# Optimization experiments

Measured on AMD Instinct MI355X. Metric: run time of the kernel, lower is better.

The kernel has to match this reference:

```python
import jax, jax.numpy as jnp
import numpy as np

B, T, C, H = 256, 256, 384, 64  # batch, seq (== block_size), n_embd, head_size


def setup_inputs() -> dict:
    key = jax.random.key(0)
    kx, kk, kq, kv = jax.random.split(key, 4)
    scale = C ** -0.5
    x = jax.random.normal(kx, (B, T, C), dtype=jnp.float32)
    Wk = jax.random.normal(kk, (C, H), dtype=jnp.float32) * scale
    Wq = jax.random.normal(kq, (C, H), dtype=jnp.float32) * scale
    Wv = jax.random.normal(kv, (C, H), dtype=jnp.float32) * scale
    return {"x": x, "Wk": Wk, "Wq": Wq, "Wv": Wv}


def reference(x, Wk, Wq, Wv):
    # Single causal self-attention head (x_kv=None path). Dropout is eval-mode (identity).
    Tn = x.shape[1]
    k = x @ Wk            # [B, T, H]
    q = x @ Wq            # [B, T, H]
    v = x @ Wv            # [B, T, H]
    inv_sqrt_d = k.shape[-1] ** -0.5
    wei = jnp.einsum('bth,bsh->bts', q, k) * inv_sqrt_d  # [B, T, T]
    causal = jnp.tril(jnp.ones((Tn, Tn), dtype=bool))
    wei = jnp.where(causal, wei, -jnp.inf)
    wei = jax.nn.softmax(wei, axis=-1)
    out = jnp.einsum('bts,bsh->bth', wei, v)             # [B, T, H]
    return out
```

## Files before the change

kernel.cpp:

```cpp
#include <hip/hip_runtime.h>

#define BATCH 256
#define SEQ   256
#define CDIM  384
#define HDIM  64

typedef __attribute__((ext_vector_type(8))) short bf16x8;
typedef __attribute__((ext_vector_type(4))) float f32x4;

__device__ __forceinline__ unsigned f2bf(float f) {
  union { float f; unsigned u; } v; v.f = f;
  unsigned r = v.u + 0x7FFFu + ((v.u >> 16) & 1u);
  return r >> 16;
}

__global__ void wtrans_kernel(const float* __restrict__ Wk, const float* __restrict__ Wq,
                              const float* __restrict__ Wv, unsigned short* __restrict__ WTf) {
  int gid = blockIdx.x * 256 + threadIdx.x;
  if (gid >= 192 * CDIM) return;
  int n = gid / CDIM, kk = gid - n * CDIM;
  const float* W = (n < 64) ? Wq : (n < 128) ? Wk : Wv;
  int nt = n >> 4, ln = n & 15, ks = kk >> 5, sub = (kk >> 3) & 3, j = kk & 7;
  int lane = ln + 16 * sub;
  WTf[(((size_t)ks * 12 + nt) * 64 + lane) * 8 + j] =
      (unsigned short)f2bf(W[kk * HDIM + (n & 63)]);
}

__global__ __launch_bounds__(1024, 4) void fused_kernel(
    const float* __restrict__ x, const unsigned short* __restrict__ WTf,
    float* __restrict__ out) {
  __shared__ __align__(16) unsigned short lds[73728];
  const int tid = threadIdx.x, b = blockIdx.x;
  const int w = tid >> 6, lane = tid & 63;
  const int ln15 = lane & 15, quad = lane >> 4;

  {
    const uint4* src = (const uint4*)WTf;
    #pragma unroll
    for (int i = 0; i < 9; ++i) {
      int c = i * 1024 + tid;
      __builtin_amdgcn_global_load_lds(
          (const __attribute__((address_space(1))) unsigned*)(src + c),
          (__attribute__((address_space(3))) unsigned*)((char*)lds + (size_t)c * 16),
          16, 0, 0);
    }
  }

  bf16x8 bx[12];
  {
    const float* xr = x + (size_t)(b * 256 + w * 16 + ln15) * CDIM + quad * 8;
    #pragma unroll
    for (int hh = 0; hh < 2; ++hh) {
      float4 A[12];
      #pragma unroll
      for (int j = 0; j < 6; ++j) {
        A[2 * j]     = *(const float4*)(xr + (hh * 6 + j) * 32);
        A[2 * j + 1] = *(const float4*)(xr + (hh * 6 + j) * 32 + 4);
      }
      #pragma unroll
      for (int j = 0; j < 6; ++j) {
        bf16x8 t;
        t[0] = (short)f2bf(A[2 * j].x);     t[1] = (short)f2bf(A[2 * j].y);
        t[2] = (short)f2bf(A[2 * j].z);     t[3] = (short)f2bf(A[2 * j].w);
        t[4] = (short)f2bf(A[2 * j + 1].x); t[5] = (short)f2bf(A[2 * j + 1].y);
        t[6] = (short)f2bf(A[2 * j + 1].z); t[7] = (short)f2bf(A[2 * j + 1].w);
        bx[hh * 6 + j] = t;
      }
    }
  }

  __syncthreads();

  f32x4 acc[12];
  #pragma unroll
  for (int nt = 0; nt < 12; ++nt) acc[nt] = (f32x4){0.f, 0.f, 0.f, 0.f};

  #pragma unroll
  for (int ks = 0; ks < 12; ++ks) {
    #pragma unroll
    for (int nt = 0; nt < 12; ++nt) {
      bf16x8 aw = *(const bf16x8*)&lds[((ks * 12 + nt) * 64 + lane) * 8];
      acc[nt] = __builtin_amdgcn_mfma_f32_16x16x32_bf16(aw, bx[ks], acc[nt], 0, 0, 0);
    }
  }

  __syncthreads();

  unsigned short (*QL)[72]  = (unsigned short(*)[72])lds;
  unsigned short (*KL)[72]  = (unsigned short(*)[72])(lds + 18432);
  unsigned short (*VT)[264] = (unsigned short(*)[264])(lds + 36864);
  unsigned short (*PL)[36]  = (unsigned short(*)[36])(lds + 53760 + w * 576);

  {
    const int trow = w * 16 + ln15;
    #pragma unroll
    for (int nt = 0; nt < 4; ++nt) {
      f32x4 a = acc[nt];
      unsigned p0 = f2bf(a[0]) | (f2bf(a[1]) << 16);
      unsigned p1 = f2bf(a[2]) | (f2bf(a[3]) << 16);
      *(uint2*)&QL[trow][nt * 16 + quad * 4] = (uint2){p0, p1};
    }
    #pragma unroll
    for (int nt = 4; nt < 8; ++nt) {
      f32x4 a = acc[nt];
      unsigned p0 = f2bf(a[0]) | (f2bf(a[1]) << 16);
      unsigned p1 = f2bf(a[2]) | (f2bf(a[3]) << 16);
      *(uint2*)&KL[trow][(nt - 4) * 16 + quad * 4] = (uint2){p0, p1};
    }
    #pragma unroll
    for (int nt = 8; nt < 12; ++nt) {
      f32x4 a = acc[nt];
      const int h = (nt - 8) * 16 + quad * 4;
      #pragma unroll
      for (int i = 0; i < 4; ++i)
        VT[h + i][trow] = (unsigned short)f2bf(a[i]);
    }
  }
  __syncthreads();

  {
    const int mt = w;
    const int t0 = mt * 16;
    const int NT = (mt | 1) + 1;

    bf16x8 aq[2];
    #pragma unroll
    for (int ks = 0; ks < 2; ++ks)
      aq[ks] = *(const bf16x8*)&QL[t0 + ln15][ks * 32 + quad * 8];

    float sv[16][4];
    #pragma unroll
    for (int nt = 0; nt < 16; ++nt) {
      if (nt < NT) {
        f32x4 a2 = (f32x4){0.f, 0.f, 0.f, 0.f};
        #pragma unroll
        for (int ks = 0; ks < 2; ++ks) {
          bf16x8 bf = *(const bf16x8*)&KL[nt * 16 + ln15][ks * 32 + quad * 8];
          a2 = __builtin_amdgcn_mfma_f32_16x16x32_bf16(aq[ks], bf, a2, 0, 0, 0);
        }
        int colg = nt * 16 + ln15;
        #pragma unroll
        for (int i = 0; i < 4; ++i) {
          int rowg = t0 + quad * 4 + i;
          sv[nt][i] = (colg <= rowg) ? a2[i] * 0.125f : -3.0e38f;
        }
      }
    }
    float mx[4] = {-3.0e38f, -3.0e38f, -3.0e38f, -3.0e38f};
    #pragma unroll
    for (int nt = 0; nt < 16; ++nt)
      if (nt < NT) {
        #pragma unroll
        for (int i = 0; i < 4; ++i) mx[i] = fmaxf(mx[i], sv[nt][i]);
      }
    #pragma unroll
    for (int i = 0; i < 4; ++i) {
      mx[i] = fmaxf(mx[i], __shfl_xor(mx[i], 8, 64));
      mx[i] = fmaxf(mx[i], __shfl_xor(mx[i], 4, 64));
      mx[i] = fmaxf(mx[i], __shfl_xor(mx[i], 2, 64));
      mx[i] = fmaxf(mx[i], __shfl_xor(mx[i], 1, 64));
    }
    float sm[4] = {0.f, 0.f, 0.f, 0.f};
    #pragma unroll
    for (int nt = 0; nt < 16; ++nt)
      if (nt < NT) {
        #pragma unroll
        for (int i = 0; i < 4; ++i) {
          float e = __expf(sv[nt][i] - mx[i]);
          sv[nt][i] = e;
          sm[i] += e;
        }
      }
    #pragma unroll
    for (int i = 0; i < 4; ++i) {
      sm[i] += __shfl_xor(sm[i], 8, 64);
      sm[i] += __shfl_xor(sm[i], 4, 64);
      sm[i] += __shfl_xor(sm[i], 2, 64);
      sm[i] += __shfl_xor(sm[i], 1, 64);
    }
    float inv[4];
    #pragma unroll
    for (int i = 0; i < 4; ++i) inv[i] = 1.0f / sm[i];

    f32x4 o[4];
    #pragma unroll
    for (int ont = 0; ont < 4; ++ont) o[ont] = (f32x4){0.f, 0.f, 0.f, 0.f};

    #pragma unroll
    for (int kc = 0; kc < 8; ++kc) {
      if (kc * 2 < NT) {
        #pragma unroll
        for (int half = 0; half < 2; ++half) {
          int nt = kc * 2 + half;
          #pragma unroll
          for (int i = 0; i < 4; ++i)
            PL[quad * 4 + i][half * 16 + ln15] =
                (unsigned short)f2bf(sv[nt][i] * inv[i]);
        }
        bf16x8 pa = *(const bf16x8*)&PL[ln15][quad * 8];
        #pragma unroll
        for (int ont = 0; ont < 4; ++ont) {
          bf16x8 vb = *(const bf16x8*)&VT[ont * 16 + ln15][kc * 32 + quad * 8];
          o[ont] = __builtin_amdgcn_mfma_f32_16x16x32_bf16(pa, vb, o[ont], 0, 0, 0);
        }
      }
    }

    #pragma unroll
    for (int ont = 0; ont < 4; ++ont) {
      int h = ont * 16 + ln15;
      #pragma unroll
      for (int i = 0; i < 4; ++i)
        out[(size_t)(b * 256 + t0 + quad * 4 + i) * HDIM + h] = o[ont][i];
    }
  }
}

extern "C" void kernel_launch(void* const* d_in, const int* in_sizes, int n_in,
                              void* d_out, int out_size, void* d_ws, size_t ws_size,
                              hipStream_t stream) {
  const float* x  = (const float*)d_in[0];
  const float* Wk = (const float*)d_in[1];
  const float* Wq = (const float*)d_in[2];
  const float* Wv = (const float*)d_in[3];
  float* out = (float*)d_out;

  unsigned short* WTf = (unsigned short*)d_ws;

  wtrans_kernel<<<(192 * CDIM + 255) / 256, 256, 0, stream>>>(Wk, Wq, Wv, WTf);
  fused_kernel<<<256, 1024, 0, stream>>>(x, WTf, out);
}
```

Measured before the change: 181.3 us.

## Stream x through LDS via async DMA and load projection weights in halves

Replaces the upfront register load and conversion of each wave's x rows with per-K-chunk asynchronous global-to-LDS copies. The copies are double-buffered in a swizzled per-wave staging area and interleaved with the QKV projection MFMAs. The bf16 weight tile is now loaded in two halves into a smaller LDS region, with a block barrier and full drain between halves. The goal is to overlap x fetch latency with compute and cut register pressure from holding all of x in registers. The cost is more manual waitcnt and barrier synchronisation, plus a stall when the second weight half is loaded.

```diff
diff --git a/kernel.cpp b/kernel.cpp
--- a/kernel.cpp
+++ b/kernel.cpp
@@ -29,60 +29,109 @@
 __global__ __launch_bounds__(1024, 4) void fused_kernel(
     const float* __restrict__ x, const unsigned short* __restrict__ WTf,
     float* __restrict__ out) {
-  __shared__ __align__(16) unsigned short lds[73728];
+  __shared__ __align__(16) unsigned short lds[69632];
   const int tid = threadIdx.x, b = blockIdx.x;
   const int w = tid >> 6, lane = tid & 63;
   const int ln15 = lane & 15, quad = lane >> 4;
 
   {
-    const uint4* src = (const uint4*)WTf;
-    #pragma unroll
-    for (int i = 0; i < 9; ++i) {
-      int c = i * 1024 + tid;
-      __builtin_amdgcn_global_load_lds(
-          (const __attribute__((address_space(1))) unsigned*)(src + c),
-          (__attribute__((address_space(3))) unsigned*)((char*)lds + (size_t)c * 16),
-          16, 0, 0);
-    }
-  }
-
-  bf16x8 bx[12];
-  {
-    const float* xr = x + (size_t)(b * 256 + w * 16 + ln15) * CDIM + quad * 8;
-    #pragma unroll
-    for (int hh = 0; hh < 2; ++hh) {
-      float4 A[12];
-      #pragma unroll
-      for (int j = 0; j < 6; ++j) {
-        A[2 * j]     = *(const float4*)(xr + (hh * 6 + j) * 32);
-        A[2 * j + 1] = *(const float4*)(xr + (hh * 6 + j) * 32 + 4);
-      }
-      #pragma unroll
-      for (int j = 0; j < 6; ++j) {
-        bf16x8 t;
-        t[0] = (short)f2bf(A[2 * j].x);     t[1] = (short)f2bf(A[2 * j].y);
-        t[2] = (short)f2bf(A[2 * j].z);     t[3] = (short)f2bf(A[2 * j].w);
-        t[4] = (short)f2bf(A[2 * j + 1].x); t[5] = (short)f2bf(A[2 * j + 1].y);
-        t[6] = (short)f2bf(A[2 * j + 1].z); t[7] = (short)f2bf(A[2 * j + 1].w);
-        bx[hh * 6 + j] = t;
-      }
-    }
-  }
-
-  __syncthreads();
+    #pragma unroll
+    for (int i = 0; i < 5; ++i) {
+      int m = i * 16 + w;
+      if (m < 72) {
+        int c = m * 64 + lane;
+        __builtin_amdgcn_global_load_lds(
+            (const __attribute__((address_space(1))) unsigned*)((const char*)WTf + (size_t)c * 16),
+            (__attribute__((address_space(3))) unsigned*)((char*)lds + (size_t)c * 16),
+            16, 0, 0);
+      }
+    }
+  }
+  __builtin_amdgcn_sched_barrier(0);
+
+  const int r0 = lane >> 3;
+  const int cgs = (lane & 7) ^ r0;
+  const char* xs0 = (const char*)x +
+      ((size_t)(b * 256 + w * 16 + r0) * CDIM + cgs * 4) * 4;
+  const char* xs1 = xs0 + (size_t)8 * CDIM * 4;
+  char* xld = (char*)lds + 73728 + w * 4096 + lane * 16;
+
+#define XDMA(K, S)                                                            \
+  __builtin_amdgcn_global_load_lds(                                           \
+      (const __attribute__((address_space(1))) unsigned*)(xs0 + (K) * 128),   \
+      (__attribute__((address_space(3))) unsigned*)(xld + (S) * 2048),        \
+      16, 0, 0);                                                              \
+  __builtin_amdgcn_global_load_lds(                                           \
+      (const __attribute__((address_space(1))) unsigned*)(xs1 + (K) * 128),   \
+      (__attribute__((address_space(3))) unsigned*)(xld + (S) * 2048 + 1024), \
+      16, 0, 0);
+
+  XDMA(0, 0)
+  __builtin_amdgcn_sched_barrier(0);
+  asm volatile("s_waitcnt vmcnt(2)" ::: "memory");
+  __builtin_amdgcn_s_barrier();
+  __builtin_amdgcn_sched_barrier(0);
+
+  const int roA = ln15 * 128 + (((2 * quad) ^ (ln15 & 7)) * 16);
+  const int roB = ln15 * 128 + ((((2 * quad) + 1) ^ (ln15 & 7)) * 16);
 
   f32x4 acc[12];
   #pragma unroll
   for (int nt = 0; nt < 12; ++nt) acc[nt] = (f32x4){0.f, 0.f, 0.f, 0.f};
 
-  #pragma unroll
-  for (int ks = 0; ks < 12; ++ks) {
-    #pragma unroll
-    for (int nt = 0; nt < 12; ++nt) {
-      bf16x8 aw = *(const bf16x8*)&lds[((ks * 12 + nt) * 64 + lane) * 8];
-      acc[nt] = __builtin_amdgcn_mfma_f32_16x16x32_bf16(aw, bx[ks], acc[nt], 0, 0, 0);
-    }
-  }
+#define PSTEP(K, KIDX, VMN, ISSUE)                                            \
+  {                                                                           \
+    ISSUE                                                                     \
+    __builtin_amdgcn_sched_barrier(0);                                        \
+    asm volatile("s_waitcnt vmcnt(" #VMN ")" ::: "memory");                   \
+    __builtin_amdgcn_sched_barrier(0);                                        \
+    const char* cb = (const char*)lds + 73728 + w * 4096 + ((K) & 1) * 2048;  \
+    float4 fa = *(const float4*)(cb + roA);                                   \
+    float4 fb = *(const float4*)(cb + roB);                                   \
+    bf16x8 t;                                                                 \
+    t[0] = (short)f2bf(fa.x); t[1] = (short)f2bf(fa.y);                       \
+    t[2] = (short)f2bf(fa.z); t[3] = (short)f2bf(fa.w);                       \
+    t[4] = (short)f2bf(fb.x); t[5] = (short)f2bf(fb.y);                       \
+    t[6] = (short)f2bf(fb.z); t[7] = (short)f2bf(fb.w);                       \
+    _Pragma("unroll")                                                         \
+    for (int nt = 0; nt < 12; ++nt) {                                         \
+      bf16x8 aw = *(const bf16x8*)&lds[(((KIDX) * 12 + nt) * 64 + lane) * 8]; \
+      acc[nt] = __builtin_amdgcn_mfma_f32_16x16x32_bf16(aw, t, acc[nt], 0, 0, 0); \
+    }                                                                         \
+  }
+
+  PSTEP(0, 0, 2, XDMA(1, 1))
+  PSTEP(1, 1, 2, XDMA(2, 0))
+  PSTEP(2, 2, 2, XDMA(3, 1))
+  PSTEP(3, 3, 2, XDMA(4, 0))
+  PSTEP(4, 4, 2, XDMA(5, 1))
+  PSTEP(5, 5, 2, XDMA(6, 0))
+
+  __builtin_amdgcn_sched_barrier(0);
+  __builtin_amdgcn_s_barrier();
+  {
+    #pragma unroll
+    for (int i = 0; i < 5; ++i) {
+      int m = i * 16 + w;
+      if (m < 72) {
+        int c = m * 64 + lane;
+        __builtin_amdgcn_global_load_lds(
+            (const __attribute__((address_space(1))) unsigned*)((const char*)WTf + 73728 + (size_t)c * 16),
+            (__attribute__((address_space(3))) unsigned*)((char*)lds + (size_t)c * 16),
+            16, 0, 0);
+      }
+    }
+  }
+  asm volatile("s_waitcnt vmcnt(0)" ::: "memory");
+  __builtin_amdgcn_s_barrier();
+  __builtin_amdgcn_sched_barrier(0);
+
+  PSTEP(6,  0, 2, XDMA(7, 1))
+  PSTEP(7,  1, 2, XDMA(8, 0))
+  PSTEP(8,  2, 2, XDMA(9, 1))
+  PSTEP(9,  3, 2, XDMA(10, 0))
+  PSTEP(10, 4, 2, XDMA(11, 1))
+  PSTEP(11, 5, 0, )
 
   __syncthreads();
 
```

New measurement: 169.4 us. -6.5%, faster.

## Split each batch across two 512-thread blocks with streamed weight tiles

Applied to the files above, without the earlier changes.

Launches two 512-thread blocks per batch element instead of one 1024-thread block. The lower block handles query rows 0-127, and the upper block handles rows 128-255, recomputing K/V for the lower rows itself. The full weight matrix is no longer staged in LDS up front; each k-slice of weights is streamed in through a small double-buffered LDS window with barriers, overlapped with prefetched x loads. Q stays in registers and goes through a per-wave scratch area instead of a shared Q tile. This is meant to balance the causal work and raise parallelism, at the cost of redundant projection work in the upper block and many more barriers.

```diff
diff --git a/kernel.cpp b/kernel.cpp
--- a/kernel.cpp
+++ b/kernel.cpp
@@ -26,107 +26,131 @@
       (unsigned short)f2bf(W[kk * HDIM + (n & 63)]);
 }
 
-__global__ __launch_bounds__(1024, 4) void fused_kernel(
+__global__ __launch_bounds__(512, 4) void fused_kernel(
     const float* __restrict__ x, const unsigned short* __restrict__ WTf,
     float* __restrict__ out) {
-  __shared__ __align__(16) unsigned short lds[73728];
-  const int tid = threadIdx.x, b = blockIdx.x;
+  __shared__ __align__(16) char L[77312];
+  const int tid = threadIdx.x, bid = blockIdx.x;
+  const int b = bid & 255;
+  const bool up = bid >= 256;
   const int w = tid >> 6, lane = tid & 63;
   const int ln15 = lane & 15, quad = lane >> 4;
 
+  unsigned short (*KL)[68]  = (unsigned short(*)[68])L;
+  unsigned short (*VT)[260] = (unsigned short(*)[260])(L + 34816);
+  unsigned short (*PLw)[36] = (unsigned short(*)[36])(L + 68096 + w * 1152);
+
+#define WDMA(GREC, LREC)                                                      \
+  __builtin_amdgcn_global_load_lds(                                           \
+      (const __attribute__((address_space(1))) unsigned*)((const char*)WTf +  \
+          (size_t)(GREC) * 1024 + lane * 16),                                 \
+      (__attribute__((address_space(3))) unsigned*)(L + (LREC) * 1024 + lane * 16), \
+      16, 0, 0);
+
+#define PROJPASS(ACC, NTB, NTC, XR)                                           \
+  {                                                                           \
+    float4 Qa[2], Qb[2];                                                      \
+    Qa[0] = *(const float4*)((XR) + 0);                                       \
+    Qa[1] = *(const float4*)((XR) + 4);                                       \
+    _Pragma("unroll")                                                         \
+    for (int i = 0; i < 12; ++i) {                                            \
+      WDMA(i * 12 + (NTB) + w, w)                                             \
+      if ((NTC) == 12 && w < 4) { WDMA(i * 12 + 8 + w, 8 + w) }               \
+      if (i < 11) {                                                           \
+        if (i & 1) {                                                          \
+          Qa[0] = *(const float4*)((XR) + (i + 1) * 32);                      \
+          Qa[1] = *(const float4*)((XR) + (i + 1) * 32 + 4);                  \
+        } else {                                                              \
+          Qb[0] = *(const float4*)((XR) + (i + 1) * 32);                      \
+          Qb[1] = *(const float4*)((XR) + (i + 1) * 32 + 4);                  \
+        }                                                                     \
+      }                                                                       \
+      __builtin_amdgcn_sched_barrier(0);                                      \
+      if (i < 11) { asm volatile("s_waitcnt vmcnt(2)" ::: "memory"); }        \
+      else        { asm volatile("s_waitcnt vmcnt(0)" ::: "memory"); }        \
+      __builtin_amdgcn_s_barrier();                                           \
+      __builtin_amdgcn_sched_barrier(0);                                      \
+      {                                                                       \
+        float4 c0 = (i & 1) ? Qb[0] : Qa[0];                                  \
+        float4 c1 = (i & 1) ? Qb[1] : Qa[1];                                  \
+        bf16x8 t;                                                             \
+        t[0] = (short)f2bf(c0.x); t[1] = (short)f2bf(c0.y);                   \
+        t[2] = (short)f2bf(c0.z); t[3] = (short)f2bf(c0.w);                   \
+        t[4] = (short)f2bf(c1.x); t[5] = (short)f2bf(c1.y);                   \
+        t[6] = (short)f2bf(c1.z); t[7] = (short)f2bf(c1.w);                   \
+        _Pragma("unroll")                                                     \
+        for (int nt = 0; nt < (NTC); ++nt) {                                  \
+          bf16x8 aw = *(const bf16x8*)(L + nt * 1024 + lane * 16);            \
+          ACC[nt] = __builtin_amdgcn_mfma_f32_16x16x32_bf16(aw, t, ACC[nt], 0, 0, 0); \
+        }                                                                     \
+      }                                                                       \
+      __builtin_amdgcn_sched_barrier(0);                                      \
+      __builtin_amdgcn_s_barrier();                                           \
+      __builtin_amdgcn_sched_barrier(0);                                      \
+    }                                                                         \
+  }
+
+#define HANDKV(ACCARR, OFF, TROW)                                             \
+  {                                                                           \
+    _Pragma("unroll")                                                         \
+    for (int j = 0; j < 4; ++j) {                                             \
+      f32x4 a = ACCARR[(OFF) + j];                                            \
+      unsigned p0 = f2bf(a[0]) | (f2bf(a[1]) << 16);                          \
+      unsigned p1 = f2bf(a[2]) | (f2bf(a[3]) << 16);                          \
+      *(uint2*)&KL[TROW][j * 16 + quad * 4] = (uint2){p0, p1};                \
+    }                                                                         \
+    _Pragma("unroll")                                                         \
+    for (int j = 0; j < 4; ++j) {                                             \
+      f32x4 a = ACCARR[(OFF) + 4 + j];                                        \
+      const int h = j * 16 + quad * 4;                                        \
+      _Pragma("unroll")                                                       \
+      for (int i2 = 0; i2 < 4; ++i2)                                          \
+        VT[h + i2][TROW] = (unsigned short)f2bf(a[i2]);                       \
+    }                                                                         \
+  }
+
+  f32x4 accA[12];
+  #pragma unroll
+  for (int nt = 0; nt < 12; ++nt) accA[nt] = (f32x4){0.f, 0.f, 0.f, 0.f};
+
+  if (up) {
+    f32x4 accB[8];
+    #pragma unroll
+    for (int j = 0; j < 8; ++j) accB[j] = (f32x4){0.f, 0.f, 0.f, 0.f};
+    const float* xrB = x + ((size_t)(b * 256) + w * 16 + ln15) * CDIM + quad * 8;
+    PROJPASS(accB, 4, 8, xrB)
+    const float* xrA = xrB + (size_t)128 * CDIM;
+    PROJPASS(accA, 0, 12, xrA)
+    const int trB = w * 16 + ln15;
+    const int trA = 128 + w * 16 + ln15;
+    HANDKV(accA, 4, trA)
+    HANDKV(accB, 0, trB)
+  } else {
+    const float* xrL = x + ((size_t)(b * 256) + w * 16 + ln15) * CDIM + quad * 8;
+    PROJPASS(accA, 0, 12, xrL)
+    const int trL = w * 16 + ln15;
+    HANDKV(accA, 4, trL)
+  }
+  __syncthreads();
+
   {
-    const uint4* src = (const uint4*)WTf;
-    #pragma unroll
-    for (int i = 0; i < 9; ++i) {
-      int c = i * 1024 + tid;
-      __builtin_amdgcn_global_load_lds(
-          (const __attribute__((address_space(1))) unsigned*)(src + c),
-          (__attribute__((address_space(3))) unsigned*)((char*)lds + (size_t)c * 16),
-          16, 0, 0);
-    }
-  }
-
-  bf16x8 bx[12];
-  {
-    const float* xr = x + (size_t)(b * 256 + w * 16 + ln15) * CDIM + quad * 8;
-    #pragma unroll
-    for (int hh = 0; hh < 2; ++hh) {
-      float4 A[12];
-      #pragma unroll
-      for (int j = 0; j < 6; ++j) {
-        A[2 * j]     = *(const float4*)(xr + (hh * 6 + j) * 32);
-        A[2 * j + 1] = *(const float4*)(xr + (hh * 6 + j) * 32 + 4);
-      }
-      #pragma unroll
-      for (int j = 0; j < 6; ++j) {
-        bf16x8 t;
-        t[0] = (short)f2bf(A[2 * j].x);     t[1] = (short)f2bf(A[2 * j].y);
-        t[2] = (short)f2bf(A[2 * j].z);     t[3] = (short)f2bf(A[2 * j].w);
-        t[4] = (short)f2bf(A[2 * j + 1].x); t[5] = (short)f2bf(A[2 * j + 1].y);
-        t[6] = (short)f2bf(A[2 * j + 1].z); t[7] = (short)f2bf(A[2 * j + 1].w);
-        bx[hh * 6 + j] = t;
-      }
-    }
-  }
-
-  __syncthreads();
-
-  f32x4 acc[12];
-  #pragma unroll
-  for (int nt = 0; nt < 12; ++nt) acc[nt] = (f32x4){0.f, 0.f, 0.f, 0.f};
-
-  #pragma unroll
-  for (int ks = 0; ks < 12; ++ks) {
-    #pragma unroll
-    for (int nt = 0; nt < 12; ++nt) {
-      bf16x8 aw = *(const bf16x8*)&lds[((ks * 12 + nt) * 64 + lane) * 8];
-      acc[nt] = __builtin_amdgcn_mfma_f32_16x16x32_bf16(aw, bx[ks], acc[nt], 0, 0, 0);
-    }
-  }
-
-  __syncthreads();
-
-  unsigned short (*QL)[72]  = (unsigned short(*)[72])lds;
-  unsigned short (*KL)[72]  = (unsigned short(*)[72])(lds + 18432);
-  unsigned short (*VT)[264] = (unsigned short(*)[264])(lds + 36864);
-  unsigned short (*PL)[36]  = (unsigned short(*)[36])(lds + 53760 + w * 576);
-
-  {
-    const int trow = w * 16 + ln15;
-    #pragma unroll
-    for (int nt = 0; nt < 4; ++nt) {
-      f32x4 a = acc[nt];
-      unsigned p0 = f2bf(a[0]) | (f2bf(a[1]) << 16);
-      unsigned p1 = f2bf(a[2]) | (f2bf(a[3]) << 16);
-      *(uint2*)&QL[trow][nt * 16 + quad * 4] = (uint2){p0, p1};
-    }
-    #pragma unroll
-    for (int nt = 4; nt < 8; ++nt) {
-      f32x4 a = acc[nt];
-      unsigned p0 = f2bf(a[0]) | (f2bf(a[1]) << 16);
-      unsigned p1 = f2bf(a[2]) | (f2bf(a[3]) << 16);
-      *(uint2*)&KL[trow][(nt - 4) * 16 + quad * 4] = (uint2){p0, p1};
-    }
-    #pragma unroll
-    for (int nt = 8; nt < 12; ++nt) {
-      f32x4 a = acc[nt];
-      const int h = (nt - 8) * 16 + quad * 4;
-      #pragma unroll
-      for (int i = 0; i < 4; ++i)
-        VT[h + i][trow] = (unsigned short)f2bf(a[i]);
-    }
-  }
-  __syncthreads();
-
-  {
-    const int mt = w;
+    const int mt = up ? (8 + w) : w;
     const int t0 = mt * 16;
     const int NT = (mt | 1) + 1;
 
     bf16x8 aq[2];
     #pragma unroll
-    for (int ks = 0; ks < 2; ++ks)
-      aq[ks] = *(const bf16x8*)&QL[t0 + ln15][ks * 32 + quad * 8];
+    for (int half = 0; half < 2; ++half) {
+      #pragma unroll
+      for (int n2 = 0; n2 < 2; ++n2) {
+        f32x4 a = accA[half * 2 + n2];
+        unsigned p0 = f2bf(a[0]) | (f2bf(a[1]) << 16);
+        unsigned p1 = f2bf(a[2]) | (f2bf(a[3]) << 16);
+        *(uint2*)&PLw[ln15][n2 * 16 + quad * 4] = (uint2){p0, p1};
+      }
+      aq[half] = *(const bf16x8*)&PLw[ln15][quad * 8];
+      __builtin_amdgcn_sched_barrier(0);
+    }
 
     float sv[16][4];
     #pragma unroll
@@ -194,10 +218,10 @@
           int nt = kc * 2 + half;
           #pragma unroll
           for (int i = 0; i < 4; ++i)
-            PL[quad * 4 + i][half * 16 + ln15] =
+            PLw[quad * 4 + i][half * 16 + ln15] =
                 (unsigned short)f2bf(sv[nt][i] * inv[i]);
         }
-        bf16x8 pa = *(const bf16x8*)&PL[ln15][quad * 8];
+        bf16x8 pa = *(const bf16x8*)&PLw[ln15][quad * 8];
         #pragma unroll
         for (int ont = 0; ont < 4; ++ont) {
           bf16x8 vb = *(const bf16x8*)&VT[ont * 16 + ln15][kc * 32 + quad * 8];
@@ -228,5 +252,5 @@
   unsigned short* WTf = (unsigned short*)d_ws;
 
   wtrans_kernel<<<(192 * CDIM + 255) / 256, 256, 0, stream>>>(Wk, Wq, Wv, WTf);
-  fused_kernel<<<256, 1024, 0, stream>>>(x, WTf, out);
-}
+  fused_kernel<<<512, 512, 0, stream>>>(x, WTf, out);
+}
```

New measurement: 184.0 us. Within noise of the previous version (+1.5%).
